# Optimization experiments

Measured on AMD Instinct MI355X. Metric: run time of the kernel, lower is better.

## Reference

```python
import jax, jax.numpy as jnp
import numpy as np

jax.config.update("jax_enable_x64", True)

N = 256          # nFeatures
B = 64           # batch
C = 10.0         # capacity
DATA_SIZE = 256.0
EPS = 1e-4       # QP regularization strength (Q = EPS * I)
ITERS = 20       # fixed primal-dual interior-point iterations
SIGMA = 0.1      # centering parameter


def build_Gh(indices_male):
    """Constraints for fair_mode=1: sum x <= C, 0 <= x <= 1, fairness band on male subset."""
    m = indices_male.astype(jnp.float64)
    I = jnp.eye(N, dtype=jnp.float64)
    G = jnp.concatenate([jnp.ones((1, N)), -I, I, m[None, :], -m[None, :]], axis=0)  # [2N+3, N]
    rhs_fair = C * m.sum() / DATA_SIZE
    h = jnp.concatenate([
        jnp.array([C]),
        jnp.zeros(N, dtype=jnp.float64),
        jnp.ones(N, dtype=jnp.float64),
        jnp.array([rhs_fair + 1.0]),
        jnp.array([-rhs_fair]),
    ])  # [2N+3]
    return G, h


def solve_qp(p, G, h):
    """Batched PDIPM: min 0.5*EPS*x'x + p'x  s.t. G x <= h.  p: [B, N]."""
    nb, m = p.shape[0], G.shape[0]
    x = jnp.zeros_like(p)
    s = jnp.ones((nb, m), dtype=p.dtype)
    z = jnp.ones((nb, m), dtype=p.dtype)
    I_n = jnp.eye(N, dtype=p.dtype)

    def maxstep(v, dv):
        r = jnp.where(dv < 0, -v / dv, jnp.inf)
        return jnp.min(r, axis=1)

    def step(carry, _):
        x, s, z = carry
        mu = jnp.mean(s * z, axis=1, keepdims=True)
        rx = EPS * x + p + z @ G              # Q x + p + G^T z, [B, N]
        rs = s + x @ G.T - h                  # primal residual (G x + s - h)
        rc = s * z - SIGMA * mu               # complementarity residual
        d = z / s                             # [B, m]
        # Schur complement: Q + G^T diag(d) G, batched over B
        M = EPS * I_n + jnp.einsum('bm,mi,mj->bij', d, G, G)
        rhs = -(rx + ((-rc + z * rs) / s) @ G)
        dx = jnp.linalg.solve(M, rhs[..., None])[..., 0]
        ds = -rs - dx @ G.T
        dz = (-rc - z * ds) / s
        alpha = jnp.minimum(1.0, 0.99 * jnp.minimum(maxstep(s, ds), maxstep(z, dz)))[:, None]
        return (x + alpha * dx, s + alpha * ds, z + alpha * dz), None

    (x, s, z), _ = jax.lax.scan(step, (x, s, z), None, length=ITERS)
    return x


def setup_inputs() -> dict:
    key = jax.random.key(0)
    k1, k2 = jax.random.split(key)
    x = jax.random.normal(k1, (B, N), dtype=jnp.float32)
    indices_male = jax.random.randint(k2, (N,), 0, 2)
    return {"x": x, "indices_male": indices_male}


def reference(x, indices_male):
    G, h = build_Gh(indices_male)
    p = -x.astype(jnp.float64)                # QPFunction(Q, -inputs, ...)
    sol = solve_qp(p, G, h)
    return sol.astype(jnp.float32)
```

## Files before the change

kernel.cpp:

```cpp
#include <hip/hip_runtime.h>
#include <math.h>

#define NF 256
#define NB 64
#define M_CON 515
static constexpr double EPS_Q  = 1e-4;
static constexpr double SIGMA  = 0.1;
static constexpr double CAPC   = 10.0;
static constexpr int    ITERS  = 20;

__device__ __forceinline__ double drcp(double x) {
    double r = __builtin_amdgcn_rcp(x);
    r = fma(r, fma(-x, r, 1.0), r);
    return r;
}
__device__ __forceinline__ double drcp_fast(double x) {
    return __builtin_amdgcn_rcp(x);
}

template <int CTRL>
__device__ __forceinline__ double dpp_d(double v) {
    const int lo = __builtin_amdgcn_update_dpp(0, __double2loint(v), CTRL, 0xF, 0xF, true);
    const int hi = __builtin_amdgcn_update_dpp(0, __double2hiint(v), CTRL, 0xF, 0xF, true);
    return __hiloint2double(hi, lo);
}
__device__ __forceinline__ double bcast63(double v) {
    const int lo = __builtin_amdgcn_readlane(__double2loint(v), 63);
    const int hi = __builtin_amdgcn_readlane(__double2hiint(v), 63);
    return __hiloint2double(hi, lo);
}
__device__ __forceinline__ double wave_red_sum(double v) {
    v += dpp_d<0x121>(v);
    v += dpp_d<0x122>(v);
    v += dpp_d<0x124>(v);
    v += dpp_d<0x128>(v);
    v += dpp_d<0x142>(v);
    v += dpp_d<0x143>(v);
    return bcast63(v);
}
__device__ __forceinline__ double wave_red_max_nn(double v) {
    v = fmax(v, dpp_d<0x121>(v));
    v = fmax(v, dpp_d<0x122>(v));
    v = fmax(v, dpp_d<0x124>(v));
    v = fmax(v, dpp_d<0x128>(v));
    v = fmax(v, dpp_d<0x142>(v));
    v = fmax(v, dpp_d<0x143>(v));
    return bcast63(v);
}

__global__ __launch_bounds__(64)
void pdipm_kernel(const float* __restrict__ xin,
                  const int* __restrict__ male,
                  float* __restrict__ out) {
    const int b = blockIdx.x;
    const int lane = threadIdx.x;

    double e[4], mf[4], x[4];
    double s_lo[4], s_hi[4], z_lo[4], z_hi[4];
    double rs_lo[4], rs_hi[4];
    double msum_p = 0.0;
    #pragma unroll
    for (int k = 0; k < 4; ++k) {
        const int f = lane + 64 * k;
        const double pv = -(double)xin[b * NF + f];
        mf[k] = (double)male[f];
        msum_p += mf[k];
        e[k] = -pv;
        x[k] = 0.0;
        s_lo[k] = 1.0; s_hi[k] = 1.0;
        z_lo[k] = 1.0; z_hi[k] = 1.0;
        rs_lo[k] = 1.0;
        rs_hi[k] = 0.0;
    }
    const double nm = wave_red_sum(msum_p);
    const double rhs_fair = CAPC * nm * (1.0 / 256.0);

    double s0 = 1.0, z0 = 1.0, sA = 1.0, zA = 1.0, sB = 1.0, zB = 1.0;
    double rs0 = 1.0 - CAPC;
    double rsA = -rhs_fair;
    double rsB = 1.0 + rhs_fair;
    double musum = (double)M_CON;

    for (int it = 0; it < ITERS; ++it) {
        const double smu = SIGMA * musum * (1.0 / (double)M_CON);

        const double i_s0 = drcp(s0), i_sA = drcp(sA), i_sB = drcp(sB);
        const double i_z0 = drcp_fast(z0), i_zA = drcp_fast(zA), i_zB = drcp_fast(zB);
        const double d0 = z0 * i_s0, dA = zA * i_sA, dB = zB * i_sB;
        const double beta  = d0 * rs0 + smu * i_s0;
        const double gamma = (dA * rsA + smu * i_sA) - (dB * rsB + smu * i_sB);
        const double ia  = drcp(d0);
        const double ibb = drcp(dA + dB);

        double i_slo[4], i_shi[4], i_zlo[4], i_zhi[4];
        double d_lo[4], d_hi[4], invD[4], y[4];
        double s11_p = 0.0, s12_p = 0.0, t1_p = 0.0, t2_p = 0.0;
        #pragma unroll
        for (int k = 0; k < 4; ++k) {
            i_slo[k] = drcp(s_lo[k]);
            i_shi[k] = drcp(s_hi[k]);
            i_zlo[k] = drcp_fast(z_lo[k]);
            i_zhi[k] = drcp_fast(z_hi[k]);
            d_lo[k] = z_lo[k] * i_slo[k];
            d_hi[k] = z_hi[k] * i_shi[k];
            invD[k] = drcp(EPS_Q + d_lo[k] + d_hi[k]);
            const double rhat = e[k] + d_lo[k] * rs_lo[k] - d_hi[k] * rs_hi[k]
                              + smu * (i_slo[k] - i_shi[k]);
            y[k] = rhat * invD[k];
            s11_p += invD[k];
            s12_p += mf[k] * invD[k];
            t1_p  += y[k];
            t2_p  += mf[k] * y[k];
        }
        const double s11 = wave_red_sum(s11_p);
        const double s12 = wave_red_sum(s12_p);
        const double t1  = wave_red_sum(t1_p);
        const double t2  = wave_red_sum(t2_p);

        const double k11 = ia + s11;
        const double k22 = ibb + s12;
        const double i_det = drcp(k11 * k22 - s12 * s12);
        const double c1 = (k22 * t1 - s12 * t2) * i_det;
        const double c2 = (k11 * t2 - s12 * t1) * i_det;
        const double a1 =  ia * k22 * i_det;
        const double a2 = -ia * s12 * i_det;
        const double b1 = -ibb * s12 * i_det;
        const double b2 =  ibb * k11 * i_det;
        const double C1 = c1 + beta * a1 + gamma * b1;
        const double C2 = c2 + beta * a2 + gamma * b2;
        const double C1pC2 = C1 + C2;

        const double Sdx  = t1 - C1 * s11 - C2 * s12;
        const double Smdx = t2 - C1pC2 * s12;
        const double ds0 = -rs0 - Sdx;
        const double dsA = -rsA - Smdx;
        const double dsB = -rsB + Smdx;
        const double dz0 = smu * i_s0 - z0 - d0 * ds0;
        const double dzA = smu * i_sA - zA - dA * dsA;
        const double dzB = smu * i_sB - zB - dB * dsB;

        double dx[4], ds_lo[4], ds_hi[4], dz_lo[4], dz_hi[4];
        double dsdz_p = 0.0;
        double rmax_p = 0.0;
        #pragma unroll
        for (int k = 0; k < 4; ++k) {
            const double C12 = (mf[k] != 0.0) ? C1pC2 : C1;
            dx[k] = fma(-invD[k], C12, y[k]);
            ds_lo[k] = dx[k] - rs_lo[k];
            ds_hi[k] = -dx[k] - rs_hi[k];
            dz_lo[k] = smu * i_slo[k] - z_lo[k] - d_lo[k] * ds_lo[k];
            dz_hi[k] = smu * i_shi[k] - z_hi[k] - d_hi[k] * ds_hi[k];
            dsdz_p += ds_lo[k] * dz_lo[k] + ds_hi[k] * dz_hi[k];
            const double q1 = -ds_lo[k] * i_slo[k];
            const double q2 = -ds_hi[k] * i_shi[k];
            const double q3 = -dz_lo[k] * i_zlo[k];
            const double q4 = -dz_hi[k] * i_zhi[k];
            rmax_p = fmax(rmax_p, fmax(fmax(q1, q2), fmax(q3, q4)));
        }
        const double Sdsdz_w = wave_red_sum(dsdz_p);
        double rmax = wave_red_max_nn(rmax_p);

        rmax = fmax(rmax, fmax(-ds0 * i_s0, -dz0 * i_z0));
        rmax = fmax(rmax, fmax(-dsA * i_sA, -dzA * i_zA));
        rmax = fmax(rmax, fmax(-dsB * i_sB, -dzB * i_zB));
        const double Sdsdz = Sdsdz_w + ds0 * dz0 + dsA * dzA + dsB * dzB;

        const double alpha = fmin(1.0, 0.99 * drcp_fast(fmax(rmax, 0.99)));
        const double omA = 1.0 - alpha;

        #pragma unroll
        for (int k = 0; k < 4; ++k) {
            const double adx = alpha * dx[k];
            x[k] += adx;
            e[k] = fma(-EPS_Q, adx, e[k]);
            s_lo[k] = fma(alpha, ds_lo[k], s_lo[k]);
            s_hi[k] = fma(alpha, ds_hi[k], s_hi[k]);
            z_lo[k] = fma(alpha, dz_lo[k], z_lo[k]);
            z_hi[k] = fma(alpha, dz_hi[k], z_hi[k]);
            rs_lo[k] *= omA;
            rs_hi[k] *= omA;
        }
        s0 = fma(alpha, ds0, s0); z0 = fma(alpha, dz0, z0);
        sA = fma(alpha, dsA, sA); zA = fma(alpha, dzA, zA);
        sB = fma(alpha, dsB, sB); zB = fma(alpha, dzB, zB);
        rs0 *= omA; rsA *= omA; rsB *= omA;
        musum = musum * (1.0 - alpha * (1.0 - SIGMA)) + alpha * alpha * Sdsdz;
    }

    #pragma unroll
    for (int k = 0; k < 4; ++k)
        out[b * NF + lane + 64 * k] = (float)x[k];
}

extern "C" void kernel_launch(void* const* d_in, const int* in_sizes, int n_in,
                              void* d_out, int out_size, void* d_ws, size_t ws_size,
                              hipStream_t stream) {
    const float* xin  = (const float*)d_in[0];
    const int*   male = (const int*)d_in[1];
    float* out = (float*)d_out;
    pdipm_kernel<<<NB, 64, 0, stream>>>(xin, male, out);
}
```

Before: 73.35 us.

## Spread each batch row across four waves with shared-memory cross-wave reductions

```diff
diff --git a/kernel.cpp b/kernel.cpp
--- a/kernel.cpp
+++ b/kernel.cpp
@@ -48,31 +48,32 @@
     return bcast63(v);
 }
 
-__global__ __launch_bounds__(64)
+__global__ __launch_bounds__(256)
 void pdipm_kernel(const float* __restrict__ xin,
                   const int* __restrict__ male,
                   float* __restrict__ out) {
-    const int b = blockIdx.x;
-    const int lane = threadIdx.x;
+    const int b    = blockIdx.x;
+    const int t    = threadIdx.x;
+    const int lane = t & 63;
+    const int wv   = t >> 6;
 
-    double e[4], mf[4], x[4];
-    double s_lo[4], s_hi[4], z_lo[4], z_hi[4];
-    double rs_lo[4], rs_hi[4];
-    double msum_p = 0.0;
-    #pragma unroll
-    for (int k = 0; k < 4; ++k) {
-        const int f = lane + 64 * k;
-        const double pv = -(double)xin[b * NF + f];
-        mf[k] = (double)male[f];
-        msum_p += mf[k];
-        e[k] = -pv;
-        x[k] = 0.0;
-        s_lo[k] = 1.0; s_hi[k] = 1.0;
-        z_lo[k] = 1.0; z_hi[k] = 1.0;
-        rs_lo[k] = 1.0;
-        rs_hi[k] = 0.0;
+    __shared__ double redA[4][4];
+    __shared__ double redB[4][2];
+
+    double e, mfd, x, s_lo, s_hi, z_lo, z_hi, rs_lo, rs_hi;
+    e   = (double)xin[b * NF + t];
+    mfd = (double)male[t];
+    x = 0.0;
+    s_lo = 1.0; s_hi = 1.0; z_lo = 1.0; z_hi = 1.0;
+    rs_lo = 1.0; rs_hi = 0.0;
+
+    {
+        const double nm_w = wave_red_sum(mfd);
+        if (lane == 63) redA[wv][0] = nm_w;
+        __syncthreads();
     }
-    const double nm = wave_red_sum(msum_p);
+    const double nm = redA[0][0] + redA[1][0] + redA[2][0] + redA[3][0];
+    __syncthreads();
     const double rhs_fair = CAPC * nm * (1.0 / 256.0);
 
     double s0 = 1.0, z0 = 1.0, sA = 1.0, zA = 1.0, sB = 1.0, zB = 1.0;
@@ -92,30 +93,29 @@
         const double ia  = drcp(d0);
         const double ibb = drcp(dA + dB);
 
-        double i_slo[4], i_shi[4], i_zlo[4], i_zhi[4];
-        double d_lo[4], d_hi[4], invD[4], y[4];
-        double s11_p = 0.0, s12_p = 0.0, t1_p = 0.0, t2_p = 0.0;
-        #pragma unroll
-        for (int k = 0; k < 4; ++k) {
-            i_slo[k] = drcp(s_lo[k]);
-            i_shi[k] = drcp(s_hi[k]);
-            i_zlo[k] = drcp_fast(z_lo[k]);
-            i_zhi[k] = drcp_fast(z_hi[k]);
-            d_lo[k] = z_lo[k] * i_slo[k];
-            d_hi[k] = z_hi[k] * i_shi[k];
-            invD[k] = drcp(EPS_Q + d_lo[k] + d_hi[k]);
-            const double rhat = e[k] + d_lo[k] * rs_lo[k] - d_hi[k] * rs_hi[k]
-                              + smu * (i_slo[k] - i_shi[k]);
-            y[k] = rhat * invD[k];
-            s11_p += invD[k];
-            s12_p += mf[k] * invD[k];
-            t1_p  += y[k];
-            t2_p  += mf[k] * y[k];
+        const double i_sl = drcp(s_lo);
+        const double i_sh = drcp(s_hi);
+        const double i_zl = drcp_fast(z_lo);
+        const double i_zh = drcp_fast(z_hi);
+        const double dl = z_lo * i_sl;
+        const double dh = z_hi * i_sh;
+        const double invD = drcp(EPS_Q + dl + dh);
+        const double rhat = e + dl * rs_lo - dh * rs_hi + smu * (i_sl - i_sh);
+        const double y = rhat * invD;
+
+        const double r0 = wave_red_sum(invD);
+        const double r1 = wave_red_sum(mfd * invD);
+        const double r2 = wave_red_sum(y);
+        const double r3 = wave_red_sum(mfd * y);
+        if (lane == 63) {
+            redA[wv][0] = r0; redA[wv][1] = r1;
+            redA[wv][2] = r2; redA[wv][3] = r3;
         }
-        const double s11 = wave_red_sum(s11_p);
-        const double s12 = wave_red_sum(s12_p);
-        const double t1  = wave_red_sum(t1_p);
-        const double t2  = wave_red_sum(t2_p);
+        __syncthreads();
+        const double s11 = redA[0][0] + redA[1][0] + redA[2][0] + redA[3][0];
+        const double s12 = redA[0][1] + redA[1][1] + redA[2][1] + redA[3][1];
+        const double t1  = redA[0][2] + redA[1][2] + redA[2][2] + redA[3][2];
+        const double t2  = redA[0][3] + redA[1][3] + redA[2][3] + redA[3][3];
 
         const double k11 = ia + s11;
         const double k22 = ibb + s12;
@@ -139,47 +139,41 @@
         const double dzA = smu * i_sA - zA - dA * dsA;
         const double dzB = smu * i_sB - zB - dB * dsB;
 
-        double dx[4], ds_lo[4], ds_hi[4], dz_lo[4], dz_hi[4];
-        double dsdz_p = 0.0;
-        double rmax_p = 0.0;
-        #pragma unroll
-        for (int k = 0; k < 4; ++k) {
-            const double C12 = (mf[k] != 0.0) ? C1pC2 : C1;
-            dx[k] = fma(-invD[k], C12, y[k]);
-            ds_lo[k] = dx[k] - rs_lo[k];
-            ds_hi[k] = -dx[k] - rs_hi[k];
-            dz_lo[k] = smu * i_slo[k] - z_lo[k] - d_lo[k] * ds_lo[k];
-            dz_hi[k] = smu * i_shi[k] - z_hi[k] - d_hi[k] * ds_hi[k];
-            dsdz_p += ds_lo[k] * dz_lo[k] + ds_hi[k] * dz_hi[k];
-            const double q1 = -ds_lo[k] * i_slo[k];
-            const double q2 = -ds_hi[k] * i_shi[k];
-            const double q3 = -dz_lo[k] * i_zlo[k];
-            const double q4 = -dz_hi[k] * i_zhi[k];
-            rmax_p = fmax(rmax_p, fmax(fmax(q1, q2), fmax(q3, q4)));
-        }
-        const double Sdsdz_w = wave_red_sum(dsdz_p);
-        double rmax = wave_red_max_nn(rmax_p);
+        const double C12 = (mfd != 0.0) ? C1pC2 : C1;
+        const double dx = fma(-invD, C12, y);
+        const double ds_l = dx - rs_lo;
+        const double ds_h = -dx - rs_hi;
+        const double dz_l = smu * i_sl - z_lo - dl * ds_l;
+        const double dz_h = smu * i_sh - z_hi - dh * ds_h;
+        const double dsdz_p = ds_l * dz_l + ds_h * dz_h;
+        double rmax_p = fmax(fmax(-ds_l * i_sl, -ds_h * i_sh),
+                             fmax(-dz_l * i_zl, -dz_h * i_zh));
+
+        const double q0 = wave_red_sum(dsdz_p);
+        const double q1 = wave_red_max_nn(rmax_p);
+        if (lane == 63) { redB[wv][0] = q0; redB[wv][1] = q1; }
+        __syncthreads();
+        const double Sdsdz_f = redB[0][0] + redB[1][0] + redB[2][0] + redB[3][0];
+        double rmax = fmax(fmax(redB[0][1], redB[1][1]),
+                           fmax(redB[2][1], redB[3][1]));
 
         rmax = fmax(rmax, fmax(-ds0 * i_s0, -dz0 * i_z0));
         rmax = fmax(rmax, fmax(-dsA * i_sA, -dzA * i_zA));
         rmax = fmax(rmax, fmax(-dsB * i_sB, -dzB * i_zB));
-        const double Sdsdz = Sdsdz_w + ds0 * dz0 + dsA * dzA + dsB * dzB;
+        const double Sdsdz = Sdsdz_f + ds0 * dz0 + dsA * dzA + dsB * dzB;
 
         const double alpha = fmin(1.0, 0.99 * drcp_fast(fmax(rmax, 0.99)));
         const double omA = 1.0 - alpha;
 
-        #pragma unroll
-        for (int k = 0; k < 4; ++k) {
-            const double adx = alpha * dx[k];
-            x[k] += adx;
-            e[k] = fma(-EPS_Q, adx, e[k]);
-            s_lo[k] = fma(alpha, ds_lo[k], s_lo[k]);
-            s_hi[k] = fma(alpha, ds_hi[k], s_hi[k]);
-            z_lo[k] = fma(alpha, dz_lo[k], z_lo[k]);
-            z_hi[k] = fma(alpha, dz_hi[k], z_hi[k]);
-            rs_lo[k] *= omA;
-            rs_hi[k] *= omA;
-        }
+        const double adx = alpha * dx;
+        x += adx;
+        e = fma(-EPS_Q, adx, e);
+        s_lo = fma(alpha, ds_l, s_lo);
+        s_hi = fma(alpha, ds_h, s_hi);
+        z_lo = fma(alpha, dz_l, z_lo);
+        z_hi = fma(alpha, dz_h, z_hi);
+        rs_lo *= omA;
+        rs_hi *= omA;
         s0 = fma(alpha, ds0, s0); z0 = fma(alpha, dz0, z0);
         sA = fma(alpha, dsA, sA); zA = fma(alpha, dzA, zA);
         sB = fma(alpha, dsB, sB); zB = fma(alpha, dzB, zB);
@@ -187,9 +181,7 @@
         musum = musum * (1.0 - alpha * (1.0 - SIGMA)) + alpha * alpha * Sdsdz;
     }
 
-    #pragma unroll
-    for (int k = 0; k < 4; ++k)
-        out[b * NF + lane + 64 * k] = (float)x[k];
+    out[b * NF + t] = (float)x;
 }
 
 extern "C" void kernel_launch(void* const* d_in, const int* in_sizes, int n_in,
@@ -198,5 +190,5 @@
     const float* xin  = (const float*)d_in[0];
     const int*   male = (const int*)d_in[1];
     float* out = (float*)d_out;
-    pdipm_kernel<<<NB, 64, 0, stream>>>(xin, male, out);
+    pdipm_kernel<<<NB, 256, 0, stream>>>(xin, male, out);
 }
```

After: 74.32 us. About the same (+1.3%).
